# Optimization experiments

Measured on AMD Instinct MI355X. Metric: run time of the kernel, lower is better.

Reference implementation:

```python
import jax, jax.numpy as jnp
import numpy as np

N = 4096      # tokens
D = 4096      # input_dim
O = 4096      # output_dim
E = 8         # n_experts
R = 16        # LoRA rank (same for all experts)
K = 2         # top_k
TEMP = 1.0    # temperature
ALPHA = 1.0   # LoRA alpha


def setup_inputs() -> dict:
    key = jax.random.key(0)
    ks = jax.random.split(key, 7)
    std = 1.0 / np.sqrt(R)  # LoRALayer init: randn(input_dim, rank) * 1/sqrt(rank)
    return {
        "x": jax.random.normal(ks[0], (N, D), jnp.float32),
        "linear_w": jax.random.normal(ks[1], (D, O), jnp.float32) * 0.02,  # base nn.Linear weight (stored [in,out])
        "linear_b": jnp.zeros((O,), jnp.float32),
        "lora_A": jax.random.normal(ks[2], (E, D, R), jnp.float32) * std,
        "lora_B": jax.random.normal(ks[3], (E, R, O), jnp.float32) * 0.02,  # torch inits B to 0; randomized for nontrivial test
        "gate_w": jax.random.normal(ks[4], (E + 1, D), jnp.float32) * 0.02,  # E+1 GateLayers, each [D,1]
        "bvv": jax.random.randint(ks[5], (N, E), 0, 2, jnp.int32),  # basis_variant_binary_vector (unused in static gating)
    }


def reference(x, linear_w, linear_b, lora_A, lora_B, gate_w, bvv):
    # base path: nn.Linear
    base = x @ linear_w + linear_b                                   # [N, O]
    # all experts evaluated densely: alpha * (x @ A_e @ B_e), batched as grouped GEMMs
    lora = ALPHA * jnp.einsum("ner,ero->neo",
                              jnp.einsum("nd,edr->ner", x, lora_A),
                              lora_B)                                # [N, E, O]
    outputs = jnp.concatenate([base[:, None, :], lora], axis=1)      # [N, E+1, O]

    # static top-k gating
    logits = x @ gate_w.T                                            # [N, E+1]
    base_logits, lora_logits = logits[:, :1], logits[:, 1:]
    top_vals, top_idx = jax.lax.top_k(lora_logits, K)                # [N, K]
    rows = jnp.arange(x.shape[0])[:, None]
    # torch: zeros.scatter(top_idx, top_vals) -> non-selected experts keep logit 0.0
    lora_sparse = jnp.zeros_like(lora_logits).at[rows, top_idx].set(top_vals)
    gates = jax.nn.softmax(
        jnp.concatenate([base_logits, lora_sparse], axis=-1) / TEMP, axis=-1
    )                                                                # [N, E+1]

    return jnp.sum(outputs * gates[..., None], axis=1)               # [N, O]
```

## Files before the change

kernel.cpp:

```cpp
#include <hip/hip_runtime.h>
#include <hip/hip_bf16.h>
#include <math.h>

constexpr int Ncfg = 4096;
constexpr int Dcfg = 4096;
constexpr int Ocfg = 4096;
constexpr int Ecfg = 8;
constexpr int Rcfg = 16;
constexpr int KD   = Dcfg + Ecfg * Rcfg;
constexpr float ALPHA_C = 1.0f;
constexpr double TEMP_C = 1.0;

constexpr size_t BT_OFF = 0;
constexpr size_t AP_OFF = BT_OFF + (size_t)Ocfg * KD * 2;
constexpr size_t AT_OFF = AP_OFF + (size_t)Ncfg * KD * 2;
constexpr size_t G_OFF  = AT_OFF + (size_t)Ecfg * Rcfg * Dcfg * 2;

typedef short bf16x8 __attribute__((ext_vector_type(8)));
typedef float f32x4  __attribute__((ext_vector_type(4)));

__device__ __forceinline__ void async_load16(const __hip_bfloat16* g, __hip_bfloat16* l) {
  __builtin_amdgcn_global_load_lds((__attribute__((address_space(1))) void*)(g),
                                   (__attribute__((address_space(3))) void*)(l), 16, 0, 0);
}

__global__ __launch_bounds__(256) void prep_parallel_kernel(
    const float* __restrict__ x,  const float* __restrict__ gw,
    const float* __restrict__ W,  const float* __restrict__ lB,
    const float* __restrict__ lA,
    float* __restrict__ gates, __hip_bfloat16* __restrict__ Ap,
    __hip_bfloat16* __restrict__ BT, __hip_bfloat16* __restrict__ AT) {
  __shared__ union {
    float tile[64][65];
    float atile[256][17];
  } sm;
  const int bid = blockIdx.x;
  const int tid = threadIdx.x;

  if (bid < 512) {
    const int wave = tid >> 6, lane = tid & 63;
    const int na = bid * 8 + wave * 2, nb = na + 1;
    const float4* xa4 = (const float4*)(x + (size_t)na * Dcfg);
    const float4* xb4 = (const float4*)(x + (size_t)nb * Dcfg);
    const float4* gw4 = (const float4*)gw;
    double accA[9], accB[9];
#pragma unroll
    for (int e = 0; e < 9; e++) { accA[e] = 0.0; accB[e] = 0.0; }
    for (int i = 0; i < 16; i++) {
      int fi = lane + 64 * i;
      float4 xa = xa4[fi], xb = xb4[fi];
#pragma unroll
      for (int e = 0; e < 9; e++) {
        float4 w = gw4[e * 1024 + fi];
        accA[e] += (double)xa.x * (double)w.x + (double)xa.y * (double)w.y +
                   (double)xa.z * (double)w.z + (double)xa.w * (double)w.w;
        accB[e] += (double)xb.x * (double)w.x + (double)xb.y * (double)w.y +
                   (double)xb.z * (double)w.z + (double)xb.w * (double)w.w;
      }
    }
#pragma unroll
    for (int off = 32; off >= 1; off >>= 1) {
#pragma unroll
      for (int e = 0; e < 9; e++) {
        accA[e] += __shfl_xor(accA[e], off, 64);
        accB[e] += __shfl_xor(accB[e], off, 64);
      }
    }
    if (lane == 0) {
#pragma unroll
      for (int r = 0; r < 2; r++) {
        double lg[9];
#pragma unroll
        for (int e = 0; e < 9; e++) lg[e] = r ? accB[e] : accA[e];
        int i1 = 1;
        for (int e = 2; e <= 8; e++) if (lg[e] > lg[i1]) i1 = e;
        int i2 = -1; double v2 = -1e300;
        for (int e = 1; e <= 8; e++) if (e != i1 && lg[e] > v2) { v2 = lg[e]; i2 = e; }
        double vals[9];
        vals[0] = lg[0];
        for (int e = 1; e <= 8; e++) vals[e] = (e == i1 || e == i2) ? lg[e] : 0.0;
        double mx = vals[0];
        for (int e = 1; e < 9; e++) mx = fmax(mx, vals[e]);
        double se = 0.0, ex[9];
        for (int e = 0; e < 9; e++) { ex[e] = exp((vals[e] - mx) / TEMP_C); se += ex[e]; }
        const int n = r ? nb : na;
        for (int e = 0; e < 9; e++) gates[n * 16 + e] = (float)(ex[e] / se);
      }
    }
  } else if (bid < 6656 && bid >= 4608) {
    const int n0 = (bid - 4608) * 2;
    const float4* xr = (const float4*)(x + (size_t)n0 * Dcfg);
#pragma unroll
    for (int it = 0; it < 8; it++) {
      int fi = it * 256 + tid;
      int row = fi >> 10, c4 = fi & 1023;
      float4 v = xr[(size_t)row * 1024 + c4];
      union { ushort4 u; __hip_bfloat16 h[4]; } p;
      p.h[0] = __float2bfloat16(v.x);
      p.h[1] = __float2bfloat16(v.y);
      p.h[2] = __float2bfloat16(v.z);
      p.h[3] = __float2bfloat16(v.w);
      *(ushort4*)(Ap + (size_t)(n0 + row) * KD + 4 * c4) = p.u;
    }
  } else if (bid < 6784) {
    const float* src; int r0, c0, dstOff;
    if (bid < 4608) {
      int id = bid - 512;
      src = W; r0 = (id & 63) * 64; c0 = (id >> 6) * 64; dstOff = 0;
    } else {
      int id = bid - 6656;
      src = lB; r0 = (id & 1) * 64; c0 = (id >> 1) * 64; dstOff = Dcfg;
    }
#pragma unroll
    for (int it = 0; it < 4; it++) {
      int flat = it * 256 + tid;
      int i = flat >> 4, f = flat & 15;
      float4 v = *(const float4*)(src + (size_t)(r0 + i) * Ocfg + c0 + 4 * f);
      sm.tile[i][4 * f + 0] = v.x;
      sm.tile[i][4 * f + 1] = v.y;
      sm.tile[i][4 * f + 2] = v.z;
      sm.tile[i][4 * f + 3] = v.w;
    }
    __syncthreads();
#pragma unroll
    for (int it = 0; it < 4; it++) {
      int flat = it * 256 + tid;
      int j = flat >> 4, q = flat & 15;
      union { ushort4 u; __hip_bfloat16 h[4]; } p;
      p.h[0] = __float2bfloat16(sm.tile[4 * q + 0][j]);
      p.h[1] = __float2bfloat16(sm.tile[4 * q + 1][j]);
      p.h[2] = __float2bfloat16(sm.tile[4 * q + 2][j]);
      p.h[3] = __float2bfloat16(sm.tile[4 * q + 3][j]);
      *(ushort4*)(BT + (size_t)(c0 + j) * KD + dstOff + r0 + 4 * q) = p.u;
    }
  } else {
    const int id = bid - 6784;
    const int e = id >> 4, d0 = (id & 15) * 256;
#pragma unroll
    for (int it = 0; it < 16; it++) {
      int idx = it * 256 + tid;
      int d = idx >> 4, rr = idx & 15;
      sm.atile[d][rr] = lA[((size_t)e * Dcfg + d0 + d) * Rcfg + rr];
    }
    __syncthreads();
#pragma unroll
    for (int rr = 0; rr < Rcfg; rr++) {
      AT[((size_t)e * Rcfg + rr) * Dcfg + d0 + tid] = __float2bfloat16(sm.atile[tid][rr]);
    }
  }
}

__global__ __launch_bounds__(512) void lora_t_kernel(
    const float* __restrict__ x, const __hip_bfloat16* __restrict__ AT,
    const float* __restrict__ gates, __hip_bfloat16* __restrict__ Ap) {
  const int n0 = blockIdx.x * 16;
  const int tid = threadIdx.x;
  const int wave = tid >> 6, lane = tid & 63;
  const int m = lane & 15, quad = lane >> 4;
  const int kbase = wave * 512;

  f32x4 acc[8] = {};
  const float* xrow = x + (size_t)(n0 + m) * Dcfg + kbase + quad * 8;
  const __hip_bfloat16* atb = AT + (size_t)m * Dcfg + kbase + quad * 8;
#pragma unroll 2
  for (int kb = 0; kb < 512; kb += 32) {
    float4 x0 = *(const float4*)(xrow + kb);
    float4 x1 = *(const float4*)(xrow + kb + 4);
    union { bf16x8 v; __hip_bfloat16 h[8]; } a;
    a.h[0] = __float2bfloat16(x0.x); a.h[1] = __float2bfloat16(x0.y);
    a.h[2] = __float2bfloat16(x0.z); a.h[3] = __float2bfloat16(x0.w);
    a.h[4] = __float2bfloat16(x1.x); a.h[5] = __float2bfloat16(x1.y);
    a.h[6] = __float2bfloat16(x1.z); a.h[7] = __float2bfloat16(x1.w);
#pragma unroll
    for (int e = 0; e < Ecfg; e++) {
      bf16x8 b = *(const bf16x8*)(atb + (size_t)e * Rcfg * Dcfg + kb);
      acc[e] = __builtin_amdgcn_mfma_f32_16x16x32_bf16(a.v, b, acc[e], 0, 0, 0);
    }
  }
  __shared__ f32x4 red[8][8][64];
#pragma unroll
  for (int e = 0; e < Ecfg; e++) red[wave][e][lane] = acc[e];
  __syncthreads();
  {
    const int e = wave;
    f32x4 s = red[0][e][lane];
#pragma unroll
    for (int w = 1; w < 8; w++) s += red[w][e][lane];
#pragma unroll
    for (int rg = 0; rg < 4; rg++) {
      int nn = n0 + quad * 4 + rg;
      float g = gates[nn * 16 + 1 + e];
      Ap[(size_t)nn * KD + Dcfg + e * Rcfg + m] = __float2bfloat16(ALPHA_C * g * s[rg]);
    }
  }
}

__global__ __launch_bounds__(256) void gemm_kernel(
    const __hip_bfloat16* __restrict__ Ap, const __hip_bfloat16* __restrict__ BT,
    const float* __restrict__ gates, const float* __restrict__ bias,
    float* __restrict__ out) {
  __shared__ __hip_bfloat16 As[128 * 32];
  __shared__ __hip_bfloat16 Bs[128 * 32];
  const int tid = threadIdx.x;
  const int m0 = blockIdx.y * 128, n0 = blockIdx.x * 128;
  const int wave = tid >> 6, lane = tid & 63;
  const int wm = (wave & 1) * 64, wn = (wave >> 1) * 64;
  const int mr = lane & 15, quad = lane >> 4;

  f32x4 acc[4][4] = {};

  const int srow = tid >> 2;
  const int kc = (tid & 3) * 8;
  const __hip_bfloat16* gA0 = Ap + (size_t)(m0 + srow) * KD + kc;
  const __hip_bfloat16* gA1 = gA0 + (size_t)64 * KD;
  const __hip_bfloat16* gB0 = BT + (size_t)(n0 + srow) * KD + kc;
  const __hip_bfloat16* gB1 = gB0 + (size_t)64 * KD;
  __hip_bfloat16* lA0 = As + tid * 8;
  __hip_bfloat16* lA1 = As + 64 * 32 + tid * 8;
  __hip_bfloat16* lB0 = Bs + tid * 8;
  __hip_bfloat16* lB1 = Bs + 64 * 32 + tid * 8;

  auto kstep = [&](int kb) {
    __syncthreads();
    async_load16(gA0 + kb, lA0);
    async_load16(gA1 + kb, lA1);
    async_load16(gB0 + kb, lB0);
    async_load16(gB1 + kb, lB1);
    asm volatile("s_waitcnt vmcnt(0)" ::: "memory");
    __syncthreads();
    bf16x8 a[4], b[4];
#pragma unroll
    for (int i = 0; i < 4; i++)
      a[i] = *(const bf16x8*)&As[(wm + i * 16 + mr) * 32 + quad * 8];
#pragma unroll
    for (int j = 0; j < 4; j++)
      b[j] = *(const bf16x8*)&Bs[(wn + j * 16 + mr) * 32 + quad * 8];
#pragma unroll
    for (int i = 0; i < 4; i++)
#pragma unroll
      for (int j = 0; j < 4; j++)
        acc[i][j] = __builtin_amdgcn_mfma_f32_16x16x32_bf16(a[i], b[j], acc[i][j], 0, 0, 0);
  };

  for (int kb = 0; kb < Dcfg; kb += 32) kstep(kb);

  float g0v[4][4];
#pragma unroll
  for (int i = 0; i < 4; i++) {
    const int rowb = m0 + wm + i * 16 + quad * 4;
#pragma unroll
    for (int rg = 0; rg < 4; rg++) g0v[i][rg] = gates[(rowb + rg) * 16];
  }
#pragma unroll
  for (int i = 0; i < 4; i++)
#pragma unroll
    for (int rg = 0; rg < 4; rg++)
#pragma unroll
      for (int j = 0; j < 4; j++) acc[i][j][rg] *= g0v[i][rg];

  for (int kb = Dcfg; kb < KD; kb += 32) kstep(kb);

#pragma unroll
  for (int i = 0; i < 4; i++) {
    const int rowb = m0 + wm + i * 16 + quad * 4;
#pragma unroll
    for (int rg = 0; rg < 4; rg++) {
      const int row = rowb + rg;
#pragma unroll
      for (int j = 0; j < 4; j++) {
        const int col = n0 + wn + j * 16 + mr;
        out[(size_t)row * Ocfg + col] = acc[i][j][rg] + g0v[i][rg] * bias[col];
      }
    }
  }
}

extern "C" void kernel_launch(void* const* d_in, const int* in_sizes, int n_in,
                              void* d_out, int out_size, void* d_ws, size_t ws_size,
                              hipStream_t stream) {
  const float* x  = (const float*)d_in[0];
  const float* W  = (const float*)d_in[1];
  const float* b  = (const float*)d_in[2];
  const float* lA = (const float*)d_in[3];
  const float* lB = (const float*)d_in[4];
  const float* gw = (const float*)d_in[5];
  float* out = (float*)d_out;

  char* ws = (char*)d_ws;
  __hip_bfloat16* BT    = (__hip_bfloat16*)(ws + BT_OFF);
  __hip_bfloat16* Ap    = (__hip_bfloat16*)(ws + AP_OFF);
  __hip_bfloat16* AT    = (__hip_bfloat16*)(ws + AT_OFF);
  float*          gates = (float*)(ws + G_OFF);

  prep_parallel_kernel<<<dim3(6912), 256, 0, stream>>>(x, gw, W, lB, lA, gates, Ap, BT, AT);
  lora_t_kernel<<<dim3(Ncfg / 16), 512, 0, stream>>>(x, AT, gates, Ap);
  gemm_kernel<<<dim3(Ocfg / 128, Ncfg / 128), 256, 0, stream>>>(Ap, BT, gates, b, out);
}
```

Baseline: 424.5 us.

## Fuse x bf16 conversion with gate scaling into gating blocks, simplify GEMM loop

The gating blocks, which already read each x row, now also write the bf16 copy of x into Ap pre-scaled by the base gate g0. This removes the separate conversion blocks and the second pass over x. Because of that pre-scaling, the GEMM no longer has to scale its accumulators between the base K-range and the LoRA K-range, so it runs one uniform K loop. The cost is that g0 is applied before rounding to bf16, which changes numerics slightly, and the gating blocks now do more serial work per wave.

```diff
diff --git a/kernel.cpp b/kernel.cpp
--- a/kernel.cpp
+++ b/kernel.cpp
@@ -66,6 +66,7 @@
         accB[e] += __shfl_xor(accB[e], off, 64);
       }
     }
+    float g0A_l = 0.f, g0B_l = 0.f;
     if (lane == 0) {
 #pragma unroll
       for (int r = 0; r < 2; r++) {
@@ -85,30 +86,35 @@
         for (int e = 0; e < 9; e++) { ex[e] = exp((vals[e] - mx) / TEMP_C); se += ex[e]; }
         const int n = r ? nb : na;
         for (int e = 0; e < 9; e++) gates[n * 16 + e] = (float)(ex[e] / se);
-      }
-    }
-  } else if (bid < 6656 && bid >= 4608) {
-    const int n0 = (bid - 4608) * 2;
-    const float4* xr = (const float4*)(x + (size_t)n0 * Dcfg);
-#pragma unroll
-    for (int it = 0; it < 8; it++) {
-      int fi = it * 256 + tid;
-      int row = fi >> 10, c4 = fi & 1023;
-      float4 v = xr[(size_t)row * 1024 + c4];
+        if (r == 0) g0A_l = (float)(ex[0] / se); else g0B_l = (float)(ex[0] / se);
+      }
+    }
+    const float g0A = __shfl(g0A_l, 0, 64);
+    const float g0B = __shfl(g0B_l, 0, 64);
+    __hip_bfloat16* ara = Ap + (size_t)na * KD;
+    __hip_bfloat16* arb = Ap + (size_t)nb * KD;
+    for (int i = 0; i < 16; i++) {
+      int fi = lane + 64 * i;
+      float4 xa = xa4[fi], xb = xb4[fi];
       union { ushort4 u; __hip_bfloat16 h[4]; } p;
-      p.h[0] = __float2bfloat16(v.x);
-      p.h[1] = __float2bfloat16(v.y);
-      p.h[2] = __float2bfloat16(v.z);
-      p.h[3] = __float2bfloat16(v.w);
-      *(ushort4*)(Ap + (size_t)(n0 + row) * KD + 4 * c4) = p.u;
-    }
-  } else if (bid < 6784) {
+      p.h[0] = __float2bfloat16(g0A * xa.x);
+      p.h[1] = __float2bfloat16(g0A * xa.y);
+      p.h[2] = __float2bfloat16(g0A * xa.z);
+      p.h[3] = __float2bfloat16(g0A * xa.w);
+      *(ushort4*)(ara + (size_t)fi * 4) = p.u;
+      p.h[0] = __float2bfloat16(g0B * xb.x);
+      p.h[1] = __float2bfloat16(g0B * xb.y);
+      p.h[2] = __float2bfloat16(g0B * xb.z);
+      p.h[3] = __float2bfloat16(g0B * xb.w);
+      *(ushort4*)(arb + (size_t)fi * 4) = p.u;
+    }
+  } else if (bid < 4736) {
     const float* src; int r0, c0, dstOff;
     if (bid < 4608) {
       int id = bid - 512;
       src = W; r0 = (id & 63) * 64; c0 = (id >> 6) * 64; dstOff = 0;
     } else {
-      int id = bid - 6656;
+      int id = bid - 4608;
       src = lB; r0 = (id & 1) * 64; c0 = (id >> 1) * 64; dstOff = Dcfg;
     }
 #pragma unroll
@@ -134,7 +140,7 @@
       *(ushort4*)(BT + (size_t)(c0 + j) * KD + dstOff + r0 + 4 * q) = p.u;
     }
   } else {
-    const int id = bid - 6784;
+    const int id = bid - 4736;
     const int e = id >> 4, d0 = (id & 15) * 256;
 #pragma unroll
     for (int it = 0; it < 16; it++) {
@@ -220,7 +226,7 @@
   __hip_bfloat16* lB0 = Bs + tid * 8;
   __hip_bfloat16* lB1 = Bs + 64 * 32 + tid * 8;
 
-  auto kstep = [&](int kb) {
+  for (int kb = 0; kb < KD; kb += 32) {
     __syncthreads();
     async_load16(gA0 + kb, lA0);
     async_load16(gA1 + kb, lA1);
@@ -228,6 +234,7 @@
     async_load16(gB1 + kb, lB1);
     asm volatile("s_waitcnt vmcnt(0)" ::: "memory");
     __syncthreads();
+
     bf16x8 a[4], b[4];
 #pragma unroll
     for (int i = 0; i < 4; i++)
@@ -240,36 +247,19 @@
 #pragma unroll
       for (int j = 0; j < 4; j++)
         acc[i][j] = __builtin_amdgcn_mfma_f32_16x16x32_bf16(a[i], b[j], acc[i][j], 0, 0, 0);
-  };
-
-  for (int kb = 0; kb < Dcfg; kb += 32) kstep(kb);
-
-  float g0v[4][4];
+  }
+
 #pragma unroll
   for (int i = 0; i < 4; i++) {
     const int rowb = m0 + wm + i * 16 + quad * 4;
 #pragma unroll
-    for (int rg = 0; rg < 4; rg++) g0v[i][rg] = gates[(rowb + rg) * 16];
-  }
-#pragma unroll
-  for (int i = 0; i < 4; i++)
-#pragma unroll
-    for (int rg = 0; rg < 4; rg++)
-#pragma unroll
-      for (int j = 0; j < 4; j++) acc[i][j][rg] *= g0v[i][rg];
-
-  for (int kb = Dcfg; kb < KD; kb += 32) kstep(kb);
-
-#pragma unroll
-  for (int i = 0; i < 4; i++) {
-    const int rowb = m0 + wm + i * 16 + quad * 4;
-#pragma unroll
     for (int rg = 0; rg < 4; rg++) {
       const int row = rowb + rg;
+      const float g0 = gates[row * 16];
 #pragma unroll
       for (int j = 0; j < 4; j++) {
         const int col = n0 + wn + j * 16 + mr;
-        out[(size_t)row * Ocfg + col] = acc[i][j][rg] + g0v[i][rg] * bias[col];
+        out[(size_t)row * Ocfg + col] = acc[i][j][rg] + g0 * bias[col];
       }
     }
   }
@@ -292,7 +282,7 @@
   __hip_bfloat16* AT    = (__hip_bfloat16*)(ws + AT_OFF);
   float*          gates = (float*)(ws + G_OFF);
 
-  prep_parallel_kernel<<<dim3(6912), 256, 0, stream>>>(x, gw, W, lB, lA, gates, Ap, BT, AT);
+  prep_parallel_kernel<<<dim3(4864), 256, 0, stream>>>(x, gw, W, lB, lA, gates, Ap, BT, AT);
   lora_t_kernel<<<dim3(Ncfg / 16), 512, 0, stream>>>(x, AT, gates, Ap);
   gemm_kernel<<<dim3(Ocfg / 128, Ncfg / 128), 256, 0, stream>>>(Ap, BT, gates, b, out);
 }
```

Result: faster. 399.8 us (-5.8%).
